# Performance work log

Hardware: AMD Instinct MI355X
Metric: run time of the kernel (lower is better)

The kernel has to match this reference:

```python
import jax, jax.numpy as jnp
import numpy as np

B, S, D_MODEL, N_HEADS = 2, 256, 512, 8
HEAD_DIM = D_MODEL // N_HEADS  # 64; k.size(-1) used for scaling


def setup_inputs() -> dict:
    key = jax.random.key(0)
    ks = jax.random.split(key, 11)
    sd = 1.0 / np.sqrt(D_MODEL)
    sf = 1.0 / np.sqrt(N_HEADS * D_MODEL)
    return {
        "Q": jax.random.normal(ks[0], (B, S, D_MODEL), jnp.float32),
        "K": jax.random.normal(ks[1], (B, S, D_MODEL), jnp.float32),
        "V": jax.random.normal(ks[2], (B, S, D_MODEL), jnp.float32),
        "Wq": jax.random.normal(ks[3], (D_MODEL, D_MODEL * N_HEADS), jnp.float32) * sd,
        "bq": jax.random.normal(ks[4], (D_MODEL * N_HEADS,), jnp.float32) * sd,
        "Wk": jax.random.normal(ks[5], (D_MODEL, D_MODEL * N_HEADS), jnp.float32) * sd,
        "bk": jax.random.normal(ks[6], (D_MODEL * N_HEADS,), jnp.float32) * sd,
        "Wv": jax.random.normal(ks[7], (D_MODEL, D_MODEL * N_HEADS), jnp.float32) * sd,
        "bv": jax.random.normal(ks[8], (D_MODEL * N_HEADS,), jnp.float32) * sd,
        "Wf": jax.random.normal(ks[9], (N_HEADS * D_MODEL, D_MODEL), jnp.float32) * sf,
        "bf": jax.random.normal(ks[10], (D_MODEL,), jnp.float32) * sf,
    }


def _split_heads(x):
    # Faithful to torch: view(B, -1, n_heads, d_model//n_heads).transpose(1, 2).
    # x: (B, S, D_MODEL*N_HEADS) -> (B, N_HEADS, S*N_HEADS, HEAD_DIM)
    b = x.shape[0]
    return jnp.transpose(x.reshape(b, -1, N_HEADS, HEAD_DIM), (0, 2, 1, 3))


def reference(Q, K, V, Wq, bq, Wk, bk, Wv, bv, Wf, bf):
    q = _split_heads(Q @ Wq + bq)  # (B, H, S*H, Dh)
    k = _split_heads(K @ Wk + bk)
    v = _split_heads(V @ Wv + bv)
    scale = 1.0 / jnp.sqrt(jnp.float32(HEAD_DIM))
    scores = jnp.einsum("bhqd,bhkd->bhqk", q, k) * scale  # (B, H, S*H, S*H)
    weights = jax.nn.softmax(scores, axis=-1)
    ctx = jnp.einsum("bhqk,bhkd->bhqd", weights, v)  # (B, H, S*H, Dh)
    # transpose(1,2).view(B, -1, n_heads*d_model) -> (B, S, N_HEADS*D_MODEL)
    ctx = jnp.transpose(ctx, (0, 2, 1, 3)).reshape(Q.shape[0], -1, N_HEADS * D_MODEL)
    return ctx @ Wf + bf  # (B, S, D_MODEL)
```

## Files before the change

kernel.cpp:

```cpp
#include <hip/hip_runtime.h>
#include <hip/hip_bf16.h>


typedef __attribute__((ext_vector_type(4))) float f32x4;
typedef __attribute__((ext_vector_type(8))) short short8;
typedef __attribute__((ext_vector_type(4))) short short4v;

#define SEQ 2048
#define DH 64
#define BH 16
#define ROWS 512
#define DM 512
#define NQ 4096
#define KSPLIT 8

static __device__ __forceinline__ unsigned short f2bf(float f) {
    return __builtin_bit_cast(unsigned short, __float2bfloat16(f));
}
static __device__ __forceinline__ short4v pk4(float a, float b, float c, float d) {
    return short4v{(short)f2bf(a), (short)f2bf(b), (short)f2bf(c), (short)f2bf(d)};
}

__global__ __launch_bounds__(256) void qkv_proj_kernel(
    const float* __restrict__ Q, const float* __restrict__ K, const float* __restrict__ V,
    const float* __restrict__ Wq, const float* __restrict__ bq,
    const float* __restrict__ Wk, const float* __restrict__ bk,
    const float* __restrict__ Wv, const float* __restrict__ bv,
    unsigned short* __restrict__ q_bf, unsigned short* __restrict__ k_bf,
    unsigned short* __restrict__ vT_bf)
{
    const int mat = blockIdx.z;
    const float* X    = (mat == 0) ? Q  : (mat == 1) ? K  : V;
    const float* W    = (mat == 0) ? Wq : (mat == 1) ? Wk : Wv;
    const float* bias = (mat == 0) ? bq : (mat == 1) ? bk : bv;

    const int n0 = blockIdx.x * 64;
    const int m0 = blockIdx.y * 64;
    const int tid = threadIdx.x;
    const int w = tid >> 6, l = tid & 63;
    const int lr = l & 15, lg = l >> 4;

    __shared__ unsigned short a_lds[64][72];
    __shared__ unsigned short wt_lds[64 * 72];

    const int xr0 = tid >> 4, xc4 = (tid & 15) * 4;
    const int wn = tid & 63, wkseg = tid >> 6;
    const int wxr = (wn >> 3) & 7;

    f32x4 acc[4];
#pragma unroll
    for (int ct = 0; ct < 4; ++ct) acc[ct] = f32x4{0.f, 0.f, 0.f, 0.f};

    float4 rx[4];
    float rwv[16];

#pragma unroll
    for (int i = 0; i < 4; ++i)
        rx[i] = *reinterpret_cast<const float4*>(X + (m0 + i * 16 + xr0) * DM + xc4);
#pragma unroll
    for (int j = 0; j < 16; ++j)
        rwv[j] = W[(size_t)(wkseg * 16 + j) * NQ + n0 + wn];

    for (int t = 0; t < 8; ++t) {
#pragma unroll
        for (int i = 0; i < 4; ++i)
            *reinterpret_cast<short4v*>(&a_lds[i * 16 + xr0][xc4]) =
                pk4(rx[i].x, rx[i].y, rx[i].z, rx[i].w);
#pragma unroll
        for (int j4 = 0; j4 < 4; ++j4) {
            int kb = wkseg * 2 + (j4 >> 1);
            int off = wn * 72 + ((kb ^ wxr) << 3) + (j4 & 1) * 4;
            *reinterpret_cast<short4v*>(&wt_lds[off]) =
                pk4(rwv[j4 * 4 + 0], rwv[j4 * 4 + 1], rwv[j4 * 4 + 2], rwv[j4 * 4 + 3]);
        }
        __syncthreads();

        if (t < 7) {
            int k0 = (t + 1) * 64;
#pragma unroll
            for (int i = 0; i < 4; ++i)
                rx[i] = *reinterpret_cast<const float4*>(X + (m0 + i * 16 + xr0) * DM + k0 + xc4);
#pragma unroll
            for (int j = 0; j < 16; ++j)
                rwv[j] = W[(size_t)(k0 + wkseg * 16 + j) * NQ + n0 + wn];
        }

#pragma unroll
        for (int ks = 0; ks < 2; ++ks) {
            short8 a = *reinterpret_cast<const short8*>(&a_lds[w * 16 + lr][ks * 32 + lg * 8]);
#pragma unroll
            for (int ct = 0; ct < 4; ++ct) {
                int row = ct * 16 + lr;
                int kb = ks * 4 + lg;
                short8 b = *reinterpret_cast<const short8*>(
                    &wt_lds[row * 72 + ((kb ^ ((row >> 3) & 7)) << 3)]);
                acc[ct] = __builtin_amdgcn_mfma_f32_16x16x32_bf16(a, b, acc[ct], 0, 0, 0);
            }
        }
        __syncthreads();
    }

#pragma unroll
    for (int ct = 0; ct < 4; ++ct) {
        int c = n0 + ct * 16 + lr;
        float bv_ = bias[c];
        int h = (c >> 6) & 7, d = c & 63, c1 = c >> 9;
#pragma unroll
        for (int r = 0; r < 4; ++r) {
            int row = m0 + w * 16 + lg * 4 + r;
            int b = row >> 8, s = row & 255;
            int n = s * 8 + c1;
            unsigned short bfv = f2bf(acc[ct][r] + bv_);
            if (mat == 0)      q_bf[((b * 8 + h) * SEQ + n) * DH + d] = bfv;
            else if (mat == 1) k_bf[((b * 8 + h) * SEQ + n) * DH + d] = bfv;
            else               vT_bf[((b * 8 + h) * DH + d) * SEQ + n] = bfv;
        }
    }
}

__global__ __launch_bounds__(512, 4) void attn_kernel(
    const unsigned short* __restrict__ q_bf,
    const unsigned short* __restrict__ k_bf,
    const unsigned short* __restrict__ vT_bf,
    unsigned short* __restrict__ ctx_bf)
{
    const int bh = blockIdx.y;
    const int b = bh >> 3, h = bh & 7;
    const int n0 = blockIdx.x * 64;
    const int tid = threadIdx.x;
    const int w = tid >> 6, l = tid & 63;
    const int wq = w & 3, half = w >> 2;
    const int lr = l & 15, lg = l >> 4;
    const int gtid = tid & 255;

    const unsigned short* qb = q_bf + (size_t)bh * SEQ * DH;
    const unsigned short* kb = k_bf + (size_t)bh * SEQ * DH;
    const unsigned short* vb = vT_bf + (size_t)bh * DH * SEQ;

    __shared__ unsigned short kl[2][64][72];
    __shared__ unsigned short vl[2][64][72];
    __shared__ unsigned short pl[8][16][72];
    __shared__ float o_lds[4][16][68];
    __shared__ float l_lds[4][16];

    const int qrow = n0 + wq * 16 + lr;
    short8 aq[2];
    aq[0] = *reinterpret_cast<const short8*>(qb + qrow * DH + lg * 8);
    aq[1] = *reinterpret_cast<const short8*>(qb + qrow * DH + 32 + lg * 8);

    f32x4 o[4];
    float l_part[4];
#pragma unroll
    for (int i = 0; i < 4; ++i) {
        o[i] = f32x4{0.f, 0.f, 0.f, 0.f};
        l_part[i] = 0.f;
    }

    const int srow = gtid >> 3, sc8 = (gtid & 7) * 8;
    const int kbase0 = half * (SEQ / 2);

    short8 rk[2], rv[2];
#pragma unroll
    for (int i = 0; i < 2; ++i) {
        int row = srow + i * 32;
        rk[i] = *reinterpret_cast<const short8*>(kb + (kbase0 + row) * DH + sc8);
        rv[i] = *reinterpret_cast<const short8*>(vb + row * SEQ + kbase0 + sc8);
    }

    for (int kt = 0; kt < SEQ / 2 / 64; ++kt) {
#pragma unroll
        for (int i = 0; i < 2; ++i) {
            *reinterpret_cast<short8*>(&kl[half][srow + i * 32][sc8]) = rk[i];
            *reinterpret_cast<short8*>(&vl[half][srow + i * 32][sc8]) = rv[i];
        }
        __syncthreads();

        if (kt < SEQ / 2 / 64 - 1) {
            int kb0 = kbase0 + (kt + 1) * 64;
#pragma unroll
            for (int i = 0; i < 2; ++i) {
                int row = srow + i * 32;
                rk[i] = *reinterpret_cast<const short8*>(kb + (kb0 + row) * DH + sc8);
                rv[i] = *reinterpret_cast<const short8*>(vb + row * SEQ + kb0 + sc8);
            }
        }

        f32x4 s[4];
#pragma unroll
        for (int ct = 0; ct < 4; ++ct) s[ct] = f32x4{0.f, 0.f, 0.f, 0.f};
#pragma unroll
        for (int ks = 0; ks < 2; ++ks) {
#pragma unroll
            for (int ct = 0; ct < 4; ++ct) {
                short8 bfrag = *reinterpret_cast<const short8*>(&kl[half][ct * 16 + lr][ks * 32 + lg * 8]);
                s[ct] = __builtin_amdgcn_mfma_f32_16x16x32_bf16(aq[ks], bfrag, s[ct], 0, 0, 0);
            }
        }

#pragma unroll
        for (int r = 0; r < 4; ++r) {
            float rs = 0.f;
#pragma unroll
            for (int ct = 0; ct < 4; ++ct) {
                float p = __expf(s[ct][r] * 0.125f);
                s[ct][r] = p;
                rs += p;
            }
            l_part[r] += rs;
#pragma unroll
            for (int ct = 0; ct < 4; ++ct)
                pl[w][lg * 4 + r][ct * 16 + lr] = f2bf(s[ct][r]);
        }
        asm volatile("s_waitcnt lgkmcnt(0)" ::: "memory");
        __builtin_amdgcn_sched_barrier(0);

#pragma unroll
        for (int ks = 0; ks < 2; ++ks) {
            short8 pa = *reinterpret_cast<const short8*>(&pl[w][lr][ks * 32 + lg * 8]);
#pragma unroll
            for (int dt = 0; dt < 4; ++dt) {
                short8 vfrag = *reinterpret_cast<const short8*>(&vl[half][dt * 16 + lr][ks * 32 + lg * 8]);
                o[dt] = __builtin_amdgcn_mfma_f32_16x16x32_bf16(pa, vfrag, o[dt], 0, 0, 0);
            }
        }
        __syncthreads();
    }

    float lsum[4];
#pragma unroll
    for (int r = 0; r < 4; ++r) {
        float rs = l_part[r];
        rs += __shfl_xor(rs, 1);
        rs += __shfl_xor(rs, 2);
        rs += __shfl_xor(rs, 4);
        rs += __shfl_xor(rs, 8);
        lsum[r] = rs;
    }

    if (half == 1) {
#pragma unroll
        for (int r = 0; r < 4; ++r) {
#pragma unroll
            for (int dt = 0; dt < 4; ++dt)
                o_lds[wq][lg * 4 + r][dt * 16 + lr] = o[dt][r];
            if (lr == 0) l_lds[wq][lg * 4 + r] = lsum[r];
        }
    }
    __syncthreads();
    if (half == 0) {
#pragma unroll
        for (int r = 0; r < 4; ++r) {
            float l_tot = lsum[r] + l_lds[wq][lg * 4 + r];
            float inv = 1.f / l_tot;
            int n = n0 + wq * 16 + lg * 4 + r;
            int sp = n >> 3;
            int cbase = (n & 7) * 512 + h * 64;
#pragma unroll
            for (int dt = 0; dt < 4; ++dt) {
                float ot = o[dt][r] + o_lds[wq][lg * 4 + r][dt * 16 + lr];
                ctx_bf[((size_t)(b * 256 + sp)) * NQ + cbase + dt * 16 + lr] = f2bf(ot * inv);
            }
        }
    }
}

__global__ __launch_bounds__(256) void out_proj_splitk_kernel(
    const unsigned short* __restrict__ ctx_bf,
    const float* __restrict__ Wf,
    float* __restrict__ part)
{
    const int n0 = blockIdx.x * 64;
    const int m0 = blockIdx.y * 64;
    const int ksplit = blockIdx.z;
    const int kbase = ksplit * (NQ / KSPLIT);
    const int tid = threadIdx.x;
    const int w = tid >> 6, l = tid & 63;
    const int lr = l & 15, lg = l >> 4;

    __shared__ unsigned short a_lds[64][72];
    __shared__ unsigned short wt_lds[64 * 72];

    const int arow0 = tid >> 3, ac8 = (tid & 7) * 8;
    const int wn = tid & 63, wkseg = tid >> 6;
    const int wxr = (wn >> 3) & 7;

    f32x4 acc[4];
#pragma unroll
    for (int ct = 0; ct < 4; ++ct) acc[ct] = f32x4{0.f, 0.f, 0.f, 0.f};

    short8 ra[2];
    float rwv[16];

    {
#pragma unroll
        for (int i = 0; i < 2; ++i)
            ra[i] = *reinterpret_cast<const short8*>(
                ctx_bf + (size_t)(m0 + arow0 + i * 32) * NQ + kbase + ac8);
#pragma unroll
        for (int j = 0; j < 16; ++j)
            rwv[j] = Wf[(size_t)(kbase + wkseg * 16 + j) * DM + n0 + wn];
    }

    for (int t = 0; t < 8; ++t) {
#pragma unroll
        for (int i = 0; i < 2; ++i)
            *reinterpret_cast<short8*>(&a_lds[arow0 + i * 32][ac8]) = ra[i];
#pragma unroll
        for (int j4 = 0; j4 < 4; ++j4) {
            int kb = wkseg * 2 + (j4 >> 1);
            int off = wn * 72 + ((kb ^ wxr) << 3) + (j4 & 1) * 4;
            *reinterpret_cast<short4v*>(&wt_lds[off]) =
                pk4(rwv[j4 * 4 + 0], rwv[j4 * 4 + 1], rwv[j4 * 4 + 2], rwv[j4 * 4 + 3]);
        }
        __syncthreads();

        if (t < 7) {
            int k0 = kbase + (t + 1) * 64;
#pragma unroll
            for (int i = 0; i < 2; ++i)
                ra[i] = *reinterpret_cast<const short8*>(
                    ctx_bf + (size_t)(m0 + arow0 + i * 32) * NQ + k0 + ac8);
#pragma unroll
            for (int j = 0; j < 16; ++j)
                rwv[j] = Wf[(size_t)(k0 + wkseg * 16 + j) * DM + n0 + wn];
        }

#pragma unroll
        for (int ks = 0; ks < 2; ++ks) {
            short8 a = *reinterpret_cast<const short8*>(&a_lds[w * 16 + lr][ks * 32 + lg * 8]);
#pragma unroll
            for (int ct = 0; ct < 4; ++ct) {
                int row = ct * 16 + lr;
                int kb = ks * 4 + lg;
                short8 b = *reinterpret_cast<const short8*>(
                    &wt_lds[row * 72 + ((kb ^ ((row >> 3) & 7)) << 3)]);
                acc[ct] = __builtin_amdgcn_mfma_f32_16x16x32_bf16(a, b, acc[ct], 0, 0, 0);
            }
        }
        __syncthreads();
    }

    float* pbase = part + (size_t)ksplit * ROWS * DM;
#pragma unroll
    for (int ct = 0; ct < 4; ++ct) {
        int c = n0 + ct * 16 + lr;
#pragma unroll
        for (int r = 0; r < 4; ++r) {
            int row = m0 + w * 16 + lg * 4 + r;
            pbase[(size_t)row * DM + c] = acc[ct][r];
        }
    }
}

__global__ __launch_bounds__(256) void out_reduce_kernel(
    const float* __restrict__ part, const float* __restrict__ bf_,
    float* __restrict__ out)
{
    int i4 = blockIdx.x * 256 + threadIdx.x;
    int e = i4 * 4;
    float4 acc = *reinterpret_cast<const float4*>(bf_ + (e & (DM - 1)));
#pragma unroll
    for (int ks = 0; ks < KSPLIT; ++ks) {
        float4 p = *reinterpret_cast<const float4*>(part + (size_t)ks * ROWS * DM + e);
        acc.x += p.x; acc.y += p.y; acc.z += p.z; acc.w += p.w;
    }
    *reinterpret_cast<float4*>(out + e) = acc;
}

extern "C" void kernel_launch(void* const* d_in, const int* in_sizes, int n_in,
                              void* d_out, int out_size, void* d_ws, size_t ws_size,
                              hipStream_t stream) {
    const float* Q  = (const float*)d_in[0];
    const float* K  = (const float*)d_in[1];
    const float* V  = (const float*)d_in[2];
    const float* Wq = (const float*)d_in[3];
    const float* bq = (const float*)d_in[4];
    const float* Wk = (const float*)d_in[5];
    const float* bk = (const float*)d_in[6];
    const float* Wv = (const float*)d_in[7];
    const float* bv = (const float*)d_in[8];
    const float* Wf = (const float*)d_in[9];
    const float* bf = (const float*)d_in[10];
    float* out = (float*)d_out;

    unsigned short* q_bf  = (unsigned short*)d_ws;
    unsigned short* k_bf  = q_bf + (size_t)BH * SEQ * DH;
    unsigned short* vT_bf = k_bf + (size_t)BH * SEQ * DH;
    unsigned short* ctx_bf = vT_bf + (size_t)BH * SEQ * DH;
    float* part = (float*)d_ws;

    qkv_proj_kernel<<<dim3(NQ / 64, ROWS / 64, 3), 256, 0, stream>>>(
        Q, K, V, Wq, bq, Wk, bk, Wv, bv, q_bf, k_bf, vT_bf);
    attn_kernel<<<dim3(SEQ / 64, BH), 512, 0, stream>>>(q_bf, k_bf, vT_bf, ctx_bf);
    out_proj_splitk_kernel<<<dim3(DM / 64, ROWS / 64, KSPLIT), 256, 0, stream>>>(
        ctx_bf, Wf, part);
    out_reduce_kernel<<<dim3(ROWS * DM / 4 / 256), 256, 0, stream>>>(part, bf, out);
}
```

Baseline: 81.84 us.

## Keep P in registers via transposed MFMA and cross-lane shuffles in attention

The attention kernel now computes S^T by swapping MFMA operands, so each lane holds a row-wise slice of P. That slice is packed to bf16 with v_cvt_pk_bf16 and rearranged into the A-operand layout with two xor-shuffles, instead of a round trip through LDS with a waitcnt barrier. LDS is consolidated and reused for the final half-sum reduction, which frees shared memory and allows launch bounds to rise to 6 blocks. The final store is vectorised. The extra shuffles and selects add VALU work, and the higher occupancy target may force register spills.

```diff
diff --git a/kernel.cpp b/kernel.cpp
--- a/kernel.cpp
+++ b/kernel.cpp
@@ -5,6 +5,7 @@
 typedef __attribute__((ext_vector_type(4))) float f32x4;
 typedef __attribute__((ext_vector_type(8))) short short8;
 typedef __attribute__((ext_vector_type(4))) short short4v;
+typedef __attribute__((ext_vector_type(4))) unsigned int u32x4;
 
 #define SEQ 2048
 #define DH 64
@@ -19,6 +20,11 @@
 }
 static __device__ __forceinline__ short4v pk4(float a, float b, float c, float d) {
     return short4v{(short)f2bf(a), (short)f2bf(b), (short)f2bf(c), (short)f2bf(d)};
+}
+static __device__ __forceinline__ unsigned cvt_pk_bf16(float lo, float hi) {
+    unsigned r;
+    asm("v_cvt_pk_bf16_f32 %0, %1, %2" : "=v"(r) : "v"(lo), "v"(hi));
+    return r;
 }
 
 __global__ __launch_bounds__(256) void qkv_proj_kernel(
@@ -118,7 +124,7 @@
     }
 }
 
-__global__ __launch_bounds__(512, 4) void attn_kernel(
+__global__ __launch_bounds__(512, 6) void attn_kernel(
     const unsigned short* __restrict__ q_bf,
     const unsigned short* __restrict__ k_bf,
     const unsigned short* __restrict__ vT_bf,
@@ -137,11 +143,8 @@
     const unsigned short* kb = k_bf + (size_t)bh * SEQ * DH;
     const unsigned short* vb = vT_bf + (size_t)bh * DH * SEQ;
 
-    __shared__ unsigned short kl[2][64][72];
-    __shared__ unsigned short vl[2][64][72];
-    __shared__ unsigned short pl[8][16][72];
-    __shared__ float o_lds[4][16][68];
-    __shared__ float l_lds[4][16];
+    __shared__ __align__(16) unsigned short kvl[4][64][72];
+    __shared__ float l_red[4][16];
 
     const int qrow = n0 + wq * 16 + lr;
     short8 aq[2];
@@ -149,12 +152,9 @@
     aq[1] = *reinterpret_cast<const short8*>(qb + qrow * DH + 32 + lg * 8);
 
     f32x4 o[4];
-    float l_part[4];
-#pragma unroll
-    for (int i = 0; i < 4; ++i) {
-        o[i] = f32x4{0.f, 0.f, 0.f, 0.f};
-        l_part[i] = 0.f;
-    }
+#pragma unroll
+    for (int i = 0; i < 4; ++i) o[i] = f32x4{0.f, 0.f, 0.f, 0.f};
+    float l_part = 0.f;
 
     const int srow = gtid >> 3, sc8 = (gtid & 7) * 8;
     const int kbase0 = half * (SEQ / 2);
@@ -167,11 +167,15 @@
         rv[i] = *reinterpret_cast<const short8*>(vb + row * SEQ + kbase0 + sc8);
     }
 
+    const bool lowc  = (lg < 2);
+    const bool sendR = (lg == 0) || (lg == 3);
+    const bool oddlg = (lg & 1);
+
     for (int kt = 0; kt < SEQ / 2 / 64; ++kt) {
 #pragma unroll
         for (int i = 0; i < 2; ++i) {
-            *reinterpret_cast<short8*>(&kl[half][srow + i * 32][sc8]) = rk[i];
-            *reinterpret_cast<short8*>(&vl[half][srow + i * 32][sc8]) = rv[i];
+            *reinterpret_cast<short8*>(&kvl[half][srow + i * 32][sc8]) = rk[i];
+            *reinterpret_cast<short8*>(&kvl[2 + half][srow + i * 32][sc8]) = rv[i];
         }
         __syncthreads();
 
@@ -192,74 +196,93 @@
         for (int ks = 0; ks < 2; ++ks) {
 #pragma unroll
             for (int ct = 0; ct < 4; ++ct) {
-                short8 bfrag = *reinterpret_cast<const short8*>(&kl[half][ct * 16 + lr][ks * 32 + lg * 8]);
-                s[ct] = __builtin_amdgcn_mfma_f32_16x16x32_bf16(aq[ks], bfrag, s[ct], 0, 0, 0);
-            }
-        }
-
-#pragma unroll
-        for (int r = 0; r < 4; ++r) {
-            float rs = 0.f;
-#pragma unroll
-            for (int ct = 0; ct < 4; ++ct) {
-                float p = __expf(s[ct][r] * 0.125f);
-                s[ct][r] = p;
-                rs += p;
-            }
-            l_part[r] += rs;
-#pragma unroll
-            for (int ct = 0; ct < 4; ++ct)
-                pl[w][lg * 4 + r][ct * 16 + lr] = f2bf(s[ct][r]);
-        }
-        asm volatile("s_waitcnt lgkmcnt(0)" ::: "memory");
-        __builtin_amdgcn_sched_barrier(0);
-
+                short8 kfrag = *reinterpret_cast<const short8*>(&kvl[half][ct * 16 + lr][ks * 32 + lg * 8]);
+                s[ct] = __builtin_amdgcn_mfma_f32_16x16x32_bf16(kfrag, aq[ks], s[ct], 0, 0, 0);
+            }
+        }
+
+        float rs_t = 0.f;
+#pragma unroll
+        for (int ct = 0; ct < 4; ++ct)
+#pragma unroll
+            for (int r = 0; r < 4; ++r) {
+                float pv = exp2f(s[ct][r] * 0.18033688011112042f);
+                s[ct][r] = pv;
+                rs_t += pv;
+            }
+        l_part += rs_t;
+
+        unsigned Wp[8];
+#pragma unroll
+        for (int c = 0; c < 4; ++c) {
+            Wp[c * 2 + 0] = cvt_pk_bf16(s[c][0], s[c][1]);
+            Wp[c * 2 + 1] = cvt_pk_bf16(s[c][2], s[c][3]);
+        }
+
+        unsigned keepA[4], r1r[4];
+#pragma unroll
+        for (int a = 0; a < 2; ++a)
+#pragma unroll
+            for (int hh = 0; hh < 2; ++hh) {
+                int i = a * 2 + hh;
+                unsigned snd = lowc ? Wp[(2 * a + 1) * 2 + hh] : Wp[(2 * a) * 2 + hh];
+                keepA[i]     = lowc ? Wp[(2 * a) * 2 + hh]     : Wp[(2 * a + 1) * 2 + hh];
+                r1r[i] = (unsigned)__shfl_xor((int)snd, 32);
+            }
+        unsigned r2k[4], r2r[4];
+#pragma unroll
+        for (int i = 0; i < 4; ++i) {
+            unsigned snd = sendR ? r1r[i] : keepA[i];
+            r2k[i]       = sendR ? keepA[i] : r1r[i];
+            r2r[i] = (unsigned)__shfl_xor((int)snd, 16);
+        }
+
+        u32x4 pbu[2];
 #pragma unroll
         for (int ks = 0; ks < 2; ++ks) {
-            short8 pa = *reinterpret_cast<const short8*>(&pl[w][lr][ks * 32 + lg * 8]);
+            unsigned g0a = oddlg ? r2r[2 * ks + 0] : r2k[2 * ks + 0];
+            unsigned g0b = oddlg ? r2r[2 * ks + 1] : r2k[2 * ks + 1];
+            unsigned g1a = oddlg ? r2k[2 * ks + 0] : r2r[2 * ks + 0];
+            unsigned g1b = oddlg ? r2k[2 * ks + 1] : r2r[2 * ks + 1];
+            pbu[ks] = u32x4{g0a, g0b, g1a, g1b};
+        }
+
+#pragma unroll
+        for (int ks = 0; ks < 2; ++ks) {
+            short8 pfrag = __builtin_bit_cast(short8, pbu[ks]);
 #pragma unroll
             for (int dt = 0; dt < 4; ++dt) {
-                short8 vfrag = *reinterpret_cast<const short8*>(&vl[half][dt * 16 + lr][ks * 32 + lg * 8]);
-                o[dt] = __builtin_amdgcn_mfma_f32_16x16x32_bf16(pa, vfrag, o[dt], 0, 0, 0);
-            }
-        }
-        __syncthreads();
-    }
-
-    float lsum[4];
-#pragma unroll
-    for (int r = 0; r < 4; ++r) {
-        float rs = l_part[r];
-        rs += __shfl_xor(rs, 1);
-        rs += __shfl_xor(rs, 2);
-        rs += __shfl_xor(rs, 4);
-        rs += __shfl_xor(rs, 8);
-        lsum[r] = rs;
-    }
-
+                short8 vfrag = *reinterpret_cast<const short8*>(&kvl[2 + half][dt * 16 + lr][ks * 32 + lg * 8]);
+                o[dt] = __builtin_amdgcn_mfma_f32_16x16x32_bf16(vfrag, pfrag, o[dt], 0, 0, 0);
+            }
+        }
+        __syncthreads();
+    }
+
+    float rs = l_part;
+    rs += __shfl_xor(rs, 16);
+    rs += __shfl_xor(rs, 32);
+
+    float* o_red = (float*)&kvl[0][0][0];
+    const int orow = (wq * 16 + lr) * 72;
     if (half == 1) {
 #pragma unroll
-        for (int r = 0; r < 4; ++r) {
-#pragma unroll
-            for (int dt = 0; dt < 4; ++dt)
-                o_lds[wq][lg * 4 + r][dt * 16 + lr] = o[dt][r];
-            if (lr == 0) l_lds[wq][lg * 4 + r] = lsum[r];
-        }
+        for (int dt = 0; dt < 4; ++dt)
+            *reinterpret_cast<f32x4*>(&o_red[orow + dt * 16 + lg * 4]) = o[dt];
+        if (lg == 0) l_red[wq][lr] = rs;
     }
     __syncthreads();
     if (half == 0) {
-#pragma unroll
-        for (int r = 0; r < 4; ++r) {
-            float l_tot = lsum[r] + l_lds[wq][lg * 4 + r];
-            float inv = 1.f / l_tot;
-            int n = n0 + wq * 16 + lg * 4 + r;
-            int sp = n >> 3;
-            int cbase = (n & 7) * 512 + h * 64;
-#pragma unroll
-            for (int dt = 0; dt < 4; ++dt) {
-                float ot = o[dt][r] + o_lds[wq][lg * 4 + r][dt * 16 + lr];
-                ctx_bf[((size_t)(b * 256 + sp)) * NQ + cbase + dt * 16 + lr] = f2bf(ot * inv);
-            }
+        float inv = 1.f / (rs + l_red[wq][lr]);
+        int n = n0 + wq * 16 + lr;
+        int sp = n >> 3;
+        int cbase = (n & 7) * 512 + h * 64;
+        unsigned short* dst = ctx_bf + (size_t)(b * 256 + sp) * NQ + cbase;
+#pragma unroll
+        for (int dt = 0; dt < 4; ++dt) {
+            f32x4 oo = *reinterpret_cast<f32x4*>(&o_red[orow + dt * 16 + lg * 4]);
+            oo = (o[dt] + oo) * inv;
+            *reinterpret_cast<short4v*>(dst + dt * 16 + lg * 4) = pk4(oo[0], oo[1], oo[2], oo[3]);
         }
     }
 }
```

Measured after the change: 110.2 us. 1.35x slower.
